# Optimization experiments

Hardware: AMD Instinct MI355X
Metric: run time of the kernel (lower is better)

Reference implementation:

```python
import jax, jax.numpy as jnp
import numpy as np

# ---- constants matching init_kwargs ----
NUM_STEPS = 25
NEW_AMP = 2.0
ENC_THRESHOLD = 0.5   # encoder spike threshold
BETA = 0.95           # LIF leak
LIF_THRESHOLD = 1.0   # snntorch Leaky default threshold
FIL_LEN = 50
FIL_STD = 5.0


def _gaussian_window(M, std):
    n = np.arange(M, dtype=np.float32) - (M - 1) / 2.0
    return np.exp(-0.5 * (n / std) ** 2).astype(np.float32)


def setup_inputs() -> dict:
    key = jax.random.key(0)
    k1, k2, k3 = jax.random.split(key, 3)
    B, L, H, C = 131072, 187, 50, 5
    x = jax.random.normal(k1, (B, L), dtype=jnp.float32)
    filt = jnp.asarray(_gaussian_window(FIL_LEN, FIL_STD))
    W1 = jax.random.normal(k2, (H, L), dtype=jnp.float32) / np.sqrt(L)
    W2 = jax.random.normal(k3, (C, H), dtype=jnp.float32) / np.sqrt(H)
    return {"x": x, "filt": filt, "W1": W1, "W2": W2}


def _encoder(x, filt):
    # Gaussian smoothing (conv1d, SAME padding), amplify, threshold -> spikes
    B, L = x.shape
    K = filt.shape[0]
    y = jax.lax.conv_general_dilated(
        x[:, None, :], filt[None, None, :],
        window_strides=(1,), padding=[((K - 1) // 2, K // 2)],
        dimension_numbers=("NCH", "OIH", "NCH"))[:, 0, :]
    y = y * NEW_AMP
    return (y > ENC_THRESHOLD).astype(x.dtype)


def reference(x, filt, W1, W2):
    spikes = _encoder(x, filt)                 # [B, L], identical every step
    cur1 = spikes @ W1.T                       # [B, 50], constant over steps
    B = x.shape[0]
    mem1 = jnp.zeros((B, W1.shape[0]), x.dtype)
    mem2 = jnp.zeros((B, W2.shape[0]), x.dtype)

    def step(carry, _):
        m1, m2 = carry
        m1 = BETA * m1 + cur1
        spk1 = (m1 > LIF_THRESHOLD).astype(m1.dtype)
        m1 = m1 - spk1 * LIF_THRESHOLD         # reset-by-subtraction
        cur2 = spk1 @ W2.T
        m2 = BETA * m2 + cur2
        spk2 = (m2 > LIF_THRESHOLD).astype(m2.dtype)
        m2 = m2 - spk2 * LIF_THRESHOLD
        return (m1, m2), spk2

    (_, _), spk_rec = jax.lax.scan(step, (mem1, mem2), None, length=NUM_STEPS)
    spike_count = spikes.sum() * NUM_STEPS     # encoder.count_spike()
    return spk_rec, spike_count
```

## Files before the change

### kernel.cpp

```cpp
#include <hip/hip_runtime.h>


typedef float    f32x4 __attribute__((ext_vector_type(4)));
typedef float    f32x2 __attribute__((ext_vector_type(2)));
typedef short    s16x8 __attribute__((ext_vector_type(8)));

constexpr int L = 187;
constexpr int H = 50;
constexpr int NST = 25;
constexpr float BETA = 0.95f;
constexpr float YTH  = 0.25f;

constexpr int FT_STR = 264;
constexpr int FT_SH  = 8 * FT_STR;
constexpr int W1A_SH = 4 * 6 * 64 * 8;
constexpr int W2A_SH = 2 * 64 * 8;
constexpr int NPART  = 4096;

__device__ inline unsigned short f2bf(float f) {
    union { float f; unsigned u; } v; v.f = f;
    return (unsigned short)((v.u + 0x7FFFu + ((v.u >> 16) & 1u)) >> 16);
}

__global__ void __launch_bounds__(256) prep_frags(
    const float* __restrict__ filt, const float* __restrict__ W1,
    const float* __restrict__ W2, unsigned short* __restrict__ frags)
{
    int i = blockIdx.x * 256 + threadIdx.x;
    if (i < FT_SH) {
        int r = i / FT_STR, m = i - r * FT_STR;
        int idx = m + r - 48;
        frags[i] = (idx >= 0 && idx < 50) ? f2bf(filt[idx]) : (unsigned short)0;
    } else if (i < FT_SH + W1A_SH) {
        int i2 = i - FT_SH;
        int jj = i2 & 7, lane = (i2 >> 3) & 63, kt = (i2 >> 9) % 6, mt = i2 / (512 * 6);
        int lm = lane & 15, lk = lane >> 4;
        int h = 16 * mt + lm;
        int l = 4 * lk + (jj & 3) + 16 * (2 * kt + (jj >> 2));
        unsigned short v = 0;
        if (h < H && l < L) v = f2bf(W1[h * L + l]);
        frags[i] = v;
    } else if (i < FT_SH + W1A_SH + W2A_SH) {
        int i3 = i - FT_SH - W1A_SH;
        int jj = i3 & 7, lane = (i3 >> 3) & 63, kt = i3 >> 9;
        int lm = lane & 15, lk = lane >> 4;
        int h = 4 * lk + (jj & 3) + 16 * (2 * kt + (jj >> 2));
        unsigned short v = 0;
        if (lm < 5 && h < H) v = f2bf(W2[lm * H + h]);
        frags[i] = v;
    }
}

__global__ void __launch_bounds__(256, 4) snn_fused(
    const float* __restrict__ x,
    const unsigned short* __restrict__ frags,
    float* __restrict__ out, unsigned int* __restrict__ part, int B)
{
    __shared__ __align__(16) unsigned short ftabL[FT_SH];
    __shared__ __align__(16) unsigned short W1L[W1A_SH];
    __shared__ __align__(16) unsigned short W2L[W2A_SH];
    __shared__ unsigned int csh[4];

    const int tid = threadIdx.x;
    const int wid = tid >> 6, lane = tid & 63;
    const int lm = lane & 15, lk = lane >> 4;
    const int row = blockIdx.x * 64 + wid * 16 + lm;

    {
        const uint4* g = (const uint4*)frags;
        uint4* sF = (uint4*)ftabL;
        uint4* s1 = (uint4*)W1L;
        uint4* s2 = (uint4*)W2L;
        #pragma unroll 2
        for (int i = tid; i < 264; i += 256) sF[i] = g[i];
        #pragma unroll
        for (int i = tid; i < 1536; i += 256) s1[i] = g[264 + i];
        if (tid < 128) s2[tid] = g[264 + 1536 + tid];
    }
    __syncthreads();

    s16x8 xB[6];
    {
        const float* __restrict__ xr = x + (size_t)row * L;
        #pragma unroll
        for (int kt = 0; kt < 6; ++kt) {
            const int k0 = 32 * kt + 8 * lk;
            s16x8 v;
            if (k0 + 8 <= L) {
                float t[8];
                __builtin_memcpy(t, xr + k0, 32);
                #pragma unroll
                for (int jj = 0; jj < 8; ++jj) v[jj] = (short)f2bf(t[jj]);
            } else {
                #pragma unroll
                for (int jj = 0; jj < 8; ++jj) {
                    int k = k0 + jj;
                    v[jj] = (short)f2bf((k < L) ? xr[k] : 0.f);
                }
            }
            xB[kt] = v;
        }
    }

    const int dl = 8 * lk - lm + 72;
    unsigned int scnt = 0;
    s16x8 spkB[6];
    {
        constexpr int lo[6] = {0, 0, 1, 2, 3, 4};
        constexpr int hi[6] = {1, 2, 3, 4, 5, 5};
        #pragma unroll
        for (int p = 0; p < 6; ++p) {
            f32x4 y0 = (f32x4){0, 0, 0, 0}, y1 = (f32x4){0, 0, 0, 0};
            #pragma unroll
            for (int kt = 0; kt < 6; ++kt) {
                if (kt >= lo[p] && kt <= hi[p]) {
                    const int D0a = dl + 32 * kt - 32 * p;
                    const int D0b = D0a - 16;
                    s16x8 a0 = *(const s16x8*)&ftabL[(D0a & 7) * FT_STR + (D0a & ~7)];
                    s16x8 a1 = *(const s16x8*)&ftabL[(D0b & 7) * FT_STR + (D0b & ~7)];
                    y0 = __builtin_amdgcn_mfma_f32_16x16x32_bf16(a0, xB[kt], y0, 0, 0, 0);
                    y1 = __builtin_amdgcn_mfma_f32_16x16x32_bf16(a1, xB[kt], y1, 0, 0, 0);
                }
            }
            union { unsigned w[4]; s16x8 v; } pk;
            #pragma unroll
            for (int w = 0; w < 4; ++w) {
                float va = (w < 2) ? y0[2 * w]     : y1[2 * (w - 2)];
                float vb = (w < 2) ? y0[2 * w + 1] : y1[2 * (w - 2) + 1];
                bool s0 = va > YTH, s1 = vb > YTH;
                bool c0 = s0, c1 = s1;
                if (p == 5 && w >= 2) {
                    c0 = s0 && ((4 * lk + 2 * (w - 2))     < 11);
                    c1 = s1 && ((4 * lk + 2 * (w - 2) + 1) < 11);
                }
                scnt += (unsigned)__popcll(__ballot(c0));
                scnt += (unsigned)__popcll(__ballot(c1));
                pk.w[w] = (s0 ? 0x3F80u : 0u) | (s1 ? 0x3F800000u : 0u);
            }
            spkB[p] = pk.v;
        }
    }
    if (lane == 0) csh[wid] = scnt;
    __syncthreads();
    if (tid == 0) part[blockIdx.x] = csh[0] + csh[1] + csh[2] + csh[3];

    f32x4 cu[4];
    #pragma unroll
    for (int mt = 0; mt < 4; ++mt) cu[mt] = (f32x4){0, 0, 0, 0};
    #pragma unroll
    for (int mt = 0; mt < 4; ++mt)
        #pragma unroll
        for (int kt = 0; kt < 6; ++kt) {
            s16x8 a = *(const s16x8*)&W1L[((mt * 6 + kt) * 64 + lane) * 8];
            cu[mt] = __builtin_amdgcn_mfma_f32_16x16x32_bf16(a, spkB[kt], cu[mt], 0, 0, 0);
        }

    s16x8 w2a[2];
    #pragma unroll
    for (int kt = 0; kt < 2; ++kt)
        w2a[kt] = *(const s16x8*)&W2L[(kt * 64 + lane) * 8];

    f32x2 cup[4][2], m1p[4][2];
    #pragma unroll
    for (int mt = 0; mt < 4; ++mt) {
        cup[mt][0] = (f32x2){cu[mt][0], cu[mt][1]};
        cup[mt][1] = (f32x2){cu[mt][2], cu[mt][3]};
        m1p[mt][0] = (f32x2){0.f, 0.f};
        m1p[mt][1] = (f32x2){0.f, 0.f};
    }
    f32x4 m2 = (f32x4){0, 0, 0, 0};
    const f32x2 B2 = (f32x2){BETA, BETA};
    const f32x4 B4 = (f32x4){BETA, BETA, BETA, BETA};

    float* __restrict__ po = out + (size_t)row * 5;
    const size_t step = (size_t)B * 5;

#define STEP_M1(PW)                                                          \
    do {                                                                     \
        PW[7] = 0u;                                     \
        _Pragma("unroll")                                                    \
        for (int mt = 0; mt < 4; ++mt) {                                     \
            _Pragma("unroll")                                                \
            for (int hf = 0; hf < 2; ++hf) {                                 \
                if (mt == 3 && hf == 1) continue;                            \
                f32x2 m = B2 * m1p[mt][hf] + cup[mt][hf];                    \
                float s0 = (m[0] > 1.f) ? 1.f : 0.f;                         \
                float s1 = (m[1] > 1.f) ? 1.f : 0.f;                         \
                PW[2 * mt + hf] = __builtin_amdgcn_perm(                     \
                    __float_as_uint(s1), __float_as_uint(s0), 0x07060302u);  \
                m1p[mt][hf] = m - (f32x2){s0, s1};                           \
            }                                                                \
        }                                                                    \
    } while (0)

#define LIF_STEP(PWU, PWN, T, NEXT)                                          \
    do {                                                                     \
        union { unsigned w[4]; s16x8 v; } u0_, u1_;                          \
        u0_.w[0] = PWU[0]; u0_.w[1] = PWU[1];                                \
        u0_.w[2] = PWU[2]; u0_.w[3] = PWU[3];                                \
        u1_.w[0] = PWU[4]; u1_.w[1] = PWU[5];                                \
        u1_.w[2] = PWU[6]; u1_.w[3] = PWU[7];                                \
        f32x4 c2a = (f32x4){0, 0, 0, 0}, c2b = (f32x4){0, 0, 0, 0};          \
        c2a = __builtin_amdgcn_mfma_f32_16x16x32_bf16(w2a[0], u0_.v, c2a, 0, 0, 0); \
        c2b = __builtin_amdgcn_mfma_f32_16x16x32_bf16(w2a[1], u1_.v, c2b, 0, 0, 0); \
        if (NEXT) { STEP_M1(PWN); }                   \
        f32x4 mm = B4 * m2 + (c2a + c2b);                                    \
        f32x4 sv;                                                            \
        _Pragma("unroll")                                                    \
        for (int j = 0; j < 4; ++j) sv[j] = (mm[j] > 1.f) ? 1.f : 0.f;       \
        m2 = mm - sv;                                                        \
        float* __restrict__ pt = po + (size_t)(T) * step;                    \
        if (lk == 0) {                                                       \
            __builtin_memcpy(pt, &sv, 16);                     \
        } else if (lk == 1) {                                                \
            pt[4] = sv[0];                                        \
        }                                                                    \
    } while (0)

    unsigned pwA[8], pwB[8];
    STEP_M1(pwA);
    #pragma unroll 1
    for (int t = 0; t < NST - 1; t += 2) {
        LIF_STEP(pwA, pwB, t,     true);
        LIF_STEP(pwB, pwA, t + 1, true);
    }
    LIF_STEP(pwA, pwB, NST - 1, false);
#undef LIF_STEP
#undef STEP_M1
}

__global__ void __launch_bounds__(256) finalize_count(
    const unsigned int* __restrict__ part, int n,
    float* __restrict__ out, size_t off)
{
    __shared__ unsigned int sh[4];
    unsigned int s = 0;
    for (int i = threadIdx.x; i < n; i += 256) s += part[i];
    #pragma unroll
    for (int o = 32; o; o >>= 1) s += __shfl_down(s, o);
    if ((threadIdx.x & 63) == 0) sh[threadIdx.x >> 6] = s;
    __syncthreads();
    if (threadIdx.x == 0) {
        unsigned int t = sh[0] + sh[1] + sh[2] + sh[3];
        out[off] = (float)((double)t * 25.0);
    }
}

__global__ void __launch_bounds__(256) snn_fallback(
    const float* __restrict__ x, const float* __restrict__ filt,
    const float* __restrict__ W1, const float* __restrict__ W2,
    float* __restrict__ out, unsigned int* __restrict__ part, int B)
{
    __shared__ unsigned int csh[4];
    const int row = blockIdx.x * 256 + threadIdx.x;
    const bool valid = row < B;
    const int rr = valid ? row : (B - 1);
    const float* __restrict__ xr = x + (size_t)rr * L;
    float w[64], cur1[H];
    #pragma unroll
    for (int h = 0; h < H; ++h) cur1[h] = 0.f;
    int cntv = 0;
    #pragma unroll
    for (int i = 0; i < 64; ++i) w[i] = (i >= 24) ? xr[i - 24] : 0.f;
    #pragma unroll 1
    for (int s = 0; s < 12; ++s) {
        const int l0 = s * 15;
        #pragma unroll
        for (int j = 0; j < 15; ++j) {
            const int l = l0 + j;
            float yv = 0.f;
            #pragma unroll
            for (int k = 0; k < 50; ++k) yv = fmaf(w[j + k], filt[k], yv);
            const bool sb = yv > YTH;
            cntv += sb;
            const float sp = sb ? 1.f : 0.f;
            #pragma unroll
            for (int h = 0; h < H; ++h) cur1[h] = fmaf(sp, W1[h * L + l], cur1[h]);
        }
        #pragma unroll
        for (int i = 0; i < 49; ++i) w[i] = w[i + 15];
        #pragma unroll
        for (int d = 0; d < 15; ++d) {
            const int g = l0 + 40 + d;
            w[49 + d] = (g < L) ? xr[g] : 0.f;
        }
    }
    #pragma unroll
    for (int j = 0; j < 7; ++j) {
        const int l = 180 + j;
        float yv = 0.f;
        #pragma unroll
        for (int k = 0; k < 50; ++k) yv = fmaf(w[j + k], filt[k], yv);
        const bool sb = yv > YTH;
        cntv += sb;
        const float sp = sb ? 1.f : 0.f;
        #pragma unroll
        for (int h = 0; h < H; ++h) cur1[h] = fmaf(sp, W1[h * L + l], cur1[h]);
    }
    int wc = valid ? cntv : 0;
    #pragma unroll
    for (int off = 32; off; off >>= 1) wc += __shfl_down(wc, off);
    if ((threadIdx.x & 63) == 0) csh[threadIdx.x >> 6] = (unsigned)wc;
    __syncthreads();
    if (threadIdx.x == 0) part[blockIdx.x] = csh[0] + csh[1] + csh[2] + csh[3];
    float m1[H], m2[5];
    #pragma unroll
    for (int h = 0; h < H; ++h) m1[h] = 0.f;
    #pragma unroll
    for (int c = 0; c < 5; ++c) m2[c] = 0.f;
    #pragma unroll 1
    for (int t = 0; t < NST; ++t) {
        float c2[5] = {0, 0, 0, 0, 0};
        #pragma unroll
        for (int h = 0; h < H; ++h) {
            float m = fmaf(BETA, m1[h], cur1[h]);
            const float sp = (m > 1.f) ? 1.f : 0.f;
            m1[h] = m - sp;
            #pragma unroll
            for (int c = 0; c < 5; ++c) c2[c] = fmaf(sp, W2[c * H + h], c2[c]);
        }
        float* __restrict__ ot = out + ((size_t)t * B + rr) * 5;
        #pragma unroll
        for (int c = 0; c < 5; ++c) {
            float m = fmaf(BETA, m2[c], c2[c]);
            const float s2 = (m > 1.f) ? 1.f : 0.f;
            m2[c] = m - s2;
            if (valid) ot[c] = s2;
        }
    }
}

extern "C" void kernel_launch(void* const* d_in, const int* in_sizes, int n_in,
                              void* d_out, int out_size, void* d_ws, size_t ws_size,
                              hipStream_t stream)
{
    const float* x    = (const float*)d_in[0];
    const float* filt = (const float*)d_in[1];
    const float* W1   = (const float*)d_in[2];
    const float* W2   = (const float*)d_in[3];
    float* out        = (float*)d_out;
    const int B       = in_sizes[0] / L;

    unsigned int* part    = (unsigned int*)d_ws;
    unsigned short* frags = (unsigned short*)((char*)d_ws + NPART * 4);
    const int total_sh    = FT_SH + W1A_SH + W2A_SH;
    const size_t need     = (size_t)NPART * 4 + (size_t)total_sh * 2;

    if (ws_size >= need && (B % 64) == 0 && B / 64 <= NPART) {
        prep_frags<<<(total_sh + 255) / 256, 256, 0, stream>>>(filt, W1, W2, frags);
        snn_fused<<<B / 64, 256, 0, stream>>>(x, frags, out, part, B);
        finalize_count<<<1, 256, 0, stream>>>(part, B / 64, out, (size_t)NST * B * 5);
    } else {
        snn_fallback<<<(B + 255) / 256, 256, 0, stream>>>(x, filt, W1, W2, out, part, B);
        finalize_count<<<1, 256, 0, stream>>>(part, (B + 255) / 256, out, (size_t)NST * B * 5);
    }
}
```

Measured before the change: 56.50 us.

## Fuse spike-count finalize into main kernel via last-block atomic election

Removes the separate finalize_count launch. Each block publishes its partial spike count and atomically increments a counter, and the last block to arrive sums all partials after its LIF loop. A hipMemsetAsync is added to reset the counter, which still leaves one small launch. The change also inserts sched_barrier fences around the interleaved STEP_M1 inside the LIF step to constrain instruction scheduling.

```diff
diff --git a/kernel.cpp b/kernel.cpp
--- a/kernel.cpp
+++ b/kernel.cpp
@@ -54,12 +54,13 @@
 __global__ void __launch_bounds__(256, 4) snn_fused(
     const float* __restrict__ x,
     const unsigned short* __restrict__ frags,
-    float* __restrict__ out, unsigned int* __restrict__ part, int B)
+    float* __restrict__ out, unsigned int* __restrict__ part,
+    unsigned int* __restrict__ ctr, size_t cnt_off, int B)
 {
     __shared__ __align__(16) unsigned short ftabL[FT_SH];
     __shared__ __align__(16) unsigned short W1L[W1A_SH];
     __shared__ __align__(16) unsigned short W2L[W2A_SH];
-    __shared__ unsigned int csh[4];
+    __shared__ unsigned int csh[5];
 
     const int tid = threadIdx.x;
     const int wid = tid >> 6, lane = tid & 63;
@@ -142,7 +143,16 @@
     }
     if (lane == 0) csh[wid] = scnt;
     __syncthreads();
-    if (tid == 0) part[blockIdx.x] = csh[0] + csh[1] + csh[2] + csh[3];
+    if (tid == 0) {
+        unsigned tot = csh[0] + csh[1] + csh[2] + csh[3];
+        __hip_atomic_store(&part[blockIdx.x], tot,
+                           __ATOMIC_RELEASE, __HIP_MEMORY_SCOPE_AGENT);
+        unsigned prev = __hip_atomic_fetch_add(ctr, 1u,
+                           __ATOMIC_ACQ_REL, __HIP_MEMORY_SCOPE_AGENT);
+        csh[4] = (prev == (unsigned)(gridDim.x - 1)) ? 1u : 0u;
+    }
+    __syncthreads();
+    const bool elected = (csh[4] != 0u) && (wid == 0);
 
     f32x4 cu[4];
     #pragma unroll
@@ -203,7 +213,11 @@
         f32x4 c2a = (f32x4){0, 0, 0, 0}, c2b = (f32x4){0, 0, 0, 0};          \
         c2a = __builtin_amdgcn_mfma_f32_16x16x32_bf16(w2a[0], u0_.v, c2a, 0, 0, 0); \
         c2b = __builtin_amdgcn_mfma_f32_16x16x32_bf16(w2a[1], u1_.v, c2b, 0, 0, 0); \
-        if (NEXT) { STEP_M1(PWN); }                   \
+        if (NEXT) {                                                          \
+            __builtin_amdgcn_sched_barrier(0);         \
+            STEP_M1(PWN);                                                    \
+            __builtin_amdgcn_sched_barrier(0);        \
+        }                                                                    \
         f32x4 mm = B4 * m2 + (c2a + c2b);                                    \
         f32x4 sv;                                                            \
         _Pragma("unroll")                                                    \
@@ -227,6 +241,17 @@
     LIF_STEP(pwA, pwB, NST - 1, false);
 #undef LIF_STEP
 #undef STEP_M1
+
+    if (elected) {
+        const int nblk = (int)gridDim.x;
+        unsigned s = 0;
+        for (int i = lane; i < nblk; i += 64)
+            s += __hip_atomic_load(&part[i], __ATOMIC_RELAXED,
+                                   __HIP_MEMORY_SCOPE_AGENT);
+        #pragma unroll
+        for (int o = 32; o; o >>= 1) s += __shfl_down(s, o);
+        if (lane == 0) out[cnt_off] = (float)((double)s * 25.0);
+    }
 }
 
 __global__ void __launch_bounds__(256) finalize_count(
@@ -342,16 +367,18 @@
     const int B       = in_sizes[0] / L;
 
     unsigned int* part    = (unsigned int*)d_ws;
-    unsigned short* frags = (unsigned short*)((char*)d_ws + NPART * 4);
+    unsigned int* ctr     = (unsigned int*)((char*)d_ws + NPART * 4);
+    unsigned short* frags = (unsigned short*)((char*)d_ws + NPART * 4 + 64);
     const int total_sh    = FT_SH + W1A_SH + W2A_SH;
-    const size_t need     = (size_t)NPART * 4 + (size_t)total_sh * 2;
+    const size_t need     = (size_t)NPART * 4 + 64 + (size_t)total_sh * 2;
+    const size_t cnt_off  = (size_t)NST * B * 5;
 
     if (ws_size >= need && (B % 64) == 0 && B / 64 <= NPART) {
+        hipMemsetAsync(ctr, 0, sizeof(unsigned int), stream);
         prep_frags<<<(total_sh + 255) / 256, 256, 0, stream>>>(filt, W1, W2, frags);
-        snn_fused<<<B / 64, 256, 0, stream>>>(x, frags, out, part, B);
-        finalize_count<<<1, 256, 0, stream>>>(part, B / 64, out, (size_t)NST * B * 5);
+        snn_fused<<<B / 64, 256, 0, stream>>>(x, frags, out, part, ctr, cnt_off, B);
     } else {
         snn_fallback<<<(B + 255) / 256, 256, 0, stream>>>(x, filt, W1, W2, out, part, B);
-        finalize_count<<<1, 256, 0, stream>>>(part, (B + 255) / 256, out, (size_t)NST * B * 5);
-    }
-}
+        finalize_count<<<1, 256, 0, stream>>>(part, (B + 255) / 256, out, cnt_off);
+    }
+}
```

New measurement: 208.9 us. 3.7x slower.
